# Kernel optimization log

Measured on AMD Instinct MI355X. Metric: run time of the kernel, lower is better.

## Reference

```python
import jax, jax.numpy as jnp
import numpy as np

BATCH, SEQ, H, N = 8, 4096, 512, 64
DT_MIN, DT_MAX = 1e-3, 1e-1


def setup_inputs() -> dict:
    key = jax.random.key(0)
    k1, k2, k3, k4, k5 = jax.random.split(key, 5)
    n = jnp.arange(N, dtype=jnp.float32)
    # HiPPO-LegS diagonal: A[n,n] = -(n+1) -> log|diag(A)| = log(n+1)
    A_log = jnp.broadcast_to(jnp.log(n + 1.0), (H, N))
    Bv = jnp.broadcast_to(jnp.sqrt(2.0 * n + 1.0), (H, N))
    C = jax.random.normal(k1, (H, N), dtype=jnp.float32) * 0.01
    D = jnp.ones((H,), dtype=jnp.float32)
    log_dt = jax.random.uniform(k2, (H,), dtype=jnp.float32) * (
        np.log(DT_MAX) - np.log(DT_MIN)) + np.log(DT_MIN)
    # reverse-direction params (bidirectional)
    A_log_r = A_log
    B_r = Bv
    C_r = jax.random.normal(k3, (H, N), dtype=jnp.float32) * 0.01
    # out_bi Linear: weight [H, 2H], bias [H]
    W_bi = jax.random.normal(k4, (H, 2 * H), dtype=jnp.float32) / np.sqrt(2.0 * H)
    b_bi = jnp.zeros((H,), dtype=jnp.float32)
    u = jax.random.normal(k5, (BATCH, SEQ, H), dtype=jnp.float32)
    return {"u": u, "A_log": A_log, "Bv": Bv, "C": C, "D": D,
            "log_dt": log_dt, "A_log_r": A_log_r, "B_r": B_r, "C_r": C_r,
            "W_bi": W_bi, "b_bi": b_bi}


def _conv(u, A_log, Bp, Cp, D, log_dt):
    """Diagonal SSM as FFT convolution. u: [B, L, H]."""
    L = u.shape[1]
    dt = jnp.exp(log_dt)                      # [H]
    eA = jnp.exp(A_log)                       # [H, N]
    A_bar = jnp.exp(-dt[:, None] * eA)        # [H, N]
    B_bar = (A_bar - 1.0) / (-eA) * Bp        # [H, N]
    # log-space power kernel: A_bar^k = exp(k * log A_bar)
    logA = jnp.log(jnp.clip(A_bar, 1e-30, None))
    ks = jnp.arange(L, dtype=u.dtype)
    pows = jnp.exp(ks[None, None, :] * logA[:, :, None])   # [H, N, L]
    K = jnp.einsum('dn,dnl->dl', Cp * B_bar, pows)          # [H, L]
    n_fft = 2 * L
    u_f = jnp.fft.rfft(u, n=n_fft, axis=1)                  # [B, L+1, H] complex
    K_f = jnp.fft.rfft(K, n=n_fft, axis=-1)                 # [H, L+1]
    y = jnp.fft.irfft(u_f * K_f.T[None], n=n_fft, axis=1)[:, :L, :]
    return y + u * D


def reference(u, A_log, Bv, C, D, log_dt, A_log_r, B_r, C_r, W_bi, b_bi):
    y = _conv(u, A_log, Bv, C, D, log_dt)
    yr = jnp.flip(_conv(jnp.flip(u, 1), A_log_r, B_r, C_r, D, log_dt), 1)
    ycat = jnp.concatenate([y, yr], axis=-1)                # [B, L, 2H]
    return ycat @ W_bi.T + b_bi
```

## Files before the change

### kernel.cpp

```cpp
#include <hip/hip_runtime.h>
#include <hip/hip_bf16.h>
#include <stdint.h>

#define L_SEQ  4096
#define H_DIM  512
#define N_ST   64
#define N_B    8
#define N_CH   16
#define T_CH   256
#define K_GEMM 1024

typedef float  f32x4  __attribute__((ext_vector_type(4)));
typedef __bf16 bf16x8 __attribute__((ext_vector_type(8)));
typedef __bf16 bf16x4 __attribute__((ext_vector_type(4)));
typedef unsigned short u16x8 __attribute__((ext_vector_type(8)));
typedef unsigned long long ull;

#define GLOAD16(g, l) __builtin_amdgcn_global_load_lds( \
    (const __attribute__((address_space(1))) void*)(g), \
    (__attribute__((address_space(3))) void*)(l), 16, 0, 0)

__global__ __launch_bounds__(256) void k_ut(
    const float* __restrict__ u, __bf16* __restrict__ ut,
    const float* __restrict__ W, __bf16* __restrict__ Wbf,
    const float* __restrict__ A_log, const float* __restrict__ Bv,
    const float* __restrict__ C, const float* __restrict__ log_dt,
    const float* __restrict__ A_log_r, const float* __restrict__ B_r,
    const float* __restrict__ C_r,
    float* __restrict__ kk, float* __restrict__ pLG,
    float* __restrict__ pCB, float* __restrict__ pPW)
{
    __shared__ float tl[32][65];
    __shared__ float scb[64], slg[64];
    int blk = blockIdx.x;
    int t = threadIdx.x;

    if (blk >= 8192) {
        int dirh = blk - 8192;
        int dir  = dirh >> 9, h = dirh & 511;
        int d = t;
        if (d < 64) {
            int n = d;
            float dt = expf(log_dt[h]);
            const float* Al = dir ? A_log_r : A_log;
            const float* Bp = dir ? B_r    : Bv;
            const float* Cp = dir ? C_r    : C;
            float eA = expf(Al[h * N_ST + n]);
            float Ab = expf(-dt * eA);
            float Bb = (1.0f - Ab) / eA * Bp[h * N_ST + n];
            float cb = Cp[h * N_ST + n] * Bb;
            float lg = -dt * eA * 1.44269504088896f;
            scb[n] = cb; slg[n] = lg;
            pCB[dirh * 64 + n] = cb;
            pLG[dirh * 64 + n] = lg;
            pPW[dirh * 64 + n] = expf(-dt * eA * (float)T_CH);
        }
        __syncthreads();
        float s = 0.f;
        #pragma unroll
        for (int n = 0; n < 64; ++n) s += scb[n] * exp2f((float)d * slg[n]);
        kk[dirh * 256 + d] = s;
        return;
    }

    int lt = blk & 127, ht = (blk >> 7) & 7, b = blk >> 10;
    int ho = t & 63, li = t >> 6;
    #pragma unroll
    for (int it = 0; it < 8; ++it) {
        int l = it * 4 + li;
        tl[l][ho] = u[(size_t)(b * L_SEQ + lt * 32 + l) * H_DIM + ht * 64 + ho];
    }
    if (blk < 2048) {
        int i = blk * 256 + t;
        Wbf[i] = (__bf16)W[i];
    }
    __syncthreads();
    int hh = t >> 2, lrun = (t & 3) * 8;
    bf16x8 v;
    #pragma unroll
    for (int i = 0; i < 8; ++i) v[i] = (__bf16)tl[lrun + i][hh];
    *(bf16x8*)(ut + (size_t)(ht * 64 + hh) * 32768 + b * 4096 + lt * 32 + lrun) = v;
}

__global__ __launch_bounds__(512, 2) void k_state(
    const __bf16* __restrict__ ut, const float* __restrict__ pLG,
    const float* __restrict__ pPW, __bf16* __restrict__ S2)
{
    __shared__ __bf16 uts[16384];
    int h = blockIdx.x;
    int t = threadIdx.x;
    int lane = t & 63, w = t >> 6;
    int lr = lane & 15, lg = lane >> 4;
    int dir = w >> 2, mtile = w & 3;

    float s = pLG[(size_t)(dir * 512 + h) * 64 + mtile * 16 + lr];
    f32x4 pw4 = *(const f32x4*)(pPW + (size_t)(dir * 512 + h) * 64 + mtile * 16 + lg * 4);

    bf16x8 Mf[8];
    #pragma unroll
    for (int kk = 0; kk < 8; ++kk) {
        #pragma unroll
        for (int jj = 0; jj < 8; ++jj) {
            int j = kk * 32 + lg * 8 + jj;
            float e = dir ? (float)j : (float)(255 - j);
            Mf[kk][jj] = (__bf16)exp2f(e * s);
        }
    }

    for (int hf = 0; hf < 2; ++hf) {
        if (hf) __syncthreads();
        #pragma unroll
        for (int i = 0; i < 4; ++i) {
            int chunk = i * 512 + t;
            int col   = chunk >> 5;
            int l8    = (chunk & 31) << 3;
            int l8s   = l8 ^ ((col & 7) << 3);
            GLOAD16(ut + (size_t)h * 32768 + (hf * 64 + col) * 256 + l8s,
                    (char*)uts + chunk * 16);
        }
        __syncthreads();

        #pragma unroll
        for (int ntile = 0; ntile < 4; ++ntile) {
            f32x4 acc = {};
            #pragma unroll
            for (int kk = 0; kk < 8; ++kk) {
                int col = ntile * 16 + lr;
                bf16x8 bv = *(const bf16x8*)((char*)uts + col * 512
                             + (((kk * 4 + lg) ^ (col & 7)) << 4));
                acc = __builtin_amdgcn_mfma_f32_16x16x32_bf16(Mf[kk], bv, acc, 0, 0, 0);
            }
            f32x4 X;
            if (dir == 0) {
                f32x4 incl = acc;
                float p0 = pw4[0], p1 = pw4[1], p2 = pw4[2], p3 = pw4[3];
                #pragma unroll
                for (int st = 1; st <= 8; st <<= 1) {
                    float u0 = __shfl(incl[0], (lane - st) & 63);
                    float u1 = __shfl(incl[1], (lane - st) & 63);
                    float u2 = __shfl(incl[2], (lane - st) & 63);
                    float u3 = __shfl(incl[3], (lane - st) & 63);
                    if (lr >= st) {
                        incl[0] = fmaf(p0, u0, incl[0]);
                        incl[1] = fmaf(p1, u1, incl[1]);
                        incl[2] = fmaf(p2, u2, incl[2]);
                        incl[3] = fmaf(p3, u3, incl[3]);
                    }
                    p0 *= p0; p1 *= p1; p2 *= p2; p3 *= p3;
                }
                #pragma unroll
                for (int r = 0; r < 4; ++r) {
                    float sh = __shfl(incl[r], (lane - 1) & 63);
                    X[r] = (lr == 0) ? 0.f : sh;
                }
            } else {
                f32x4 incl = acc;
                float p0 = pw4[0], p1 = pw4[1], p2 = pw4[2], p3 = pw4[3];
                #pragma unroll
                for (int st = 1; st <= 8; st <<= 1) {
                    float u0 = __shfl(incl[0], (lane + st) & 63);
                    float u1 = __shfl(incl[1], (lane + st) & 63);
                    float u2 = __shfl(incl[2], (lane + st) & 63);
                    float u3 = __shfl(incl[3], (lane + st) & 63);
                    if (lr <= 15 - st) {
                        incl[0] = fmaf(p0, u0, incl[0]);
                        incl[1] = fmaf(p1, u1, incl[1]);
                        incl[2] = fmaf(p2, u2, incl[2]);
                        incl[3] = fmaf(p3, u3, incl[3]);
                    }
                    p0 *= p0; p1 *= p1; p2 *= p2; p3 *= p3;
                }
                #pragma unroll
                for (int r = 0; r < 4; ++r) {
                    float sh = __shfl(incl[r], (lane + 1) & 63);
                    X[r] = (lr == 15) ? 0.f : sh;
                }
            }
            int colg = hf * 64 + ntile * 16 + lr;
            int nq   = mtile * 4 + lg;
            bf16x4 o;
            #pragma unroll
            for (int r = 0; r < 4; ++r) o[r] = (__bf16)X[r];
            *(bf16x4*)(S2 + ((size_t)((dir * 512 + h) * 16 + nq) * 128 + colg) * 4) = o;
        }
    }
}

template<int DIR>
__device__ __forceinline__ void conv_body(
    int h, int t,
    const float* __restrict__ kk, const float* __restrict__ pLG,
    const float* __restrict__ pCB, const float* __restrict__ Dv,
    const __bf16* __restrict__ ut, const __bf16* __restrict__ S,
    __bf16* __restrict__ ycT,
    __bf16* uts, ull* kkq8, float* slg, float* scb)
{
    int dirh = DIR * 512 + h;
    int lane = t & 63, w = t >> 6;
    int lr = lane & 15, lg = lane >> 4;

    unsigned short* asc = (unsigned short*)uts;
    for (int i = t; i < 548; i += 512) {
        int d = DIR ? (i - 272) : (271 - i);
        float kv = (d >= 0 && d < 256) ? kk[dirh * 256 + d] : 0.f;
        asc[i] = __builtin_bit_cast(unsigned short, (__bf16)kv);
    }
    if (t < 64)       slg[t]      = pLG[dirh * 64 + t];
    else if (t < 128) scb[t - 64] = pCB[dirh * 64 + (t - 64)];
    __syncthreads();
    for (int i = t; i < 544; i += 512)
        kkq8[i] = (ull)asc[i] | ((ull)asc[i+1] << 16) | ((ull)asc[i+2] << 32)
                | ((ull)asc[i+3] << 48);
    __syncthreads();

    bf16x8 gvv[2][2];
    #pragma unroll
    for (int nt = 0; nt < 2; ++nt)
        #pragma unroll
        for (int mf = 0; mf < 2; ++mf) {
            int rt = mf ? (15 - w) : w;
            int l  = rt * 16 + lr;
            float e = DIR ? (float)(256 - l) : (float)(l + 1);
            #pragma unroll
            for (int j = 0; j < 8; ++j) {
                int n = nt * 32 + lg * 8 + j;
                gvv[nt][mf][j] = (__bf16)(scb[n] * exp2f(e * slg[n]));
            }
        }

    float Dh = Dv[h];
    const ull* kq = kkq8;

    #pragma unroll
    for (int hf = 0; hf < 2; ++hf)
        #pragma unroll
        for (int i = 0; i < 4; ++i) {
            int chunk = i * 512 + t;
            int col   = chunk >> 5;
            int l8    = (chunk & 31) << 3;
            int l8s   = l8 ^ ((col & 7) << 3);
            GLOAD16(ut + (size_t)h * 32768 + (hf * 64 + col) * 256 + l8s,
                    (char*)uts + hf * 32768 + chunk * 16);
        }
    asm volatile("s_waitcnt vmcnt(4)" ::: "memory");
    __builtin_amdgcn_sched_barrier(0);
    __builtin_amdgcn_s_barrier();
    __builtin_amdgcn_sched_barrier(0);

    #pragma unroll
    for (int hf = 0; hf < 2; ++hf) {
        if (hf) __syncthreads();
        char* ub = (char*)uts + hf * 32768;

        f32x4 acc[2][4] = {};

        #pragma unroll
        for (int mf = 0; mf < 2; ++mf) {
            int rt  = mf ? (15 - w) : w;
            int jlo = DIR ? (rt >> 1) : 0;
            int jhi = DIR ? 8 : ((rt >> 1) + 1);
            int sb  = (DIR ? 272 : 271) + lg * 8 - rt * 16 - lr;
            for (int jt = jlo; jt < jhi; ++jt) {
                bf16x8 bv[4];
                #pragma unroll
                for (int n = 0; n < 4; ++n) {
                    int col = n * 16 + lr;
                    bv[n] = *(const bf16x8*)(ub + col * 512
                              + (((jt * 4 + lg) ^ (col & 7)) << 4));
                }
                int si = sb + jt * 32;
                ull lo = kq[si], hi = kq[si + 4];
                bf16x8 av;
                ((ull*)&av)[0] = lo; ((ull*)&av)[1] = hi;
                #pragma unroll
                for (int n = 0; n < 4; ++n)
                    acc[mf][n] = __builtin_amdgcn_mfma_f32_16x16x32_bf16(av, bv[n], acc[mf][n], 0, 0, 0);
            }
        }

        #pragma unroll
        for (int nt = 0; nt < 2; ++nt) {
            bf16x8 bs[4];
            #pragma unroll
            for (int n = 0; n < 4; ++n) {
                int colg = (hf * 4 + n) * 16 + lr;
                int nq0  = nt * 8 + lg * 2;
                const __bf16* sp = S + ((size_t)((DIR * 512 + h) * 16 + nq0) * 128 + colg) * 4;
                bf16x4 s0 = *(const bf16x4*)(sp);
                bf16x4 s1 = *(const bf16x4*)(sp + 512);
                #pragma unroll
                for (int j = 0; j < 4; ++j) { bs[n][j] = s0[j]; bs[n][4 + j] = s1[j]; }
            }
            #pragma unroll
            for (int mf = 0; mf < 2; ++mf)
                #pragma unroll
                for (int n = 0; n < 4; ++n)
                    acc[mf][n] = __builtin_amdgcn_mfma_f32_16x16x32_bf16(gvv[nt][mf], bs[n], acc[mf][n], 0, 0, 0);
        }

        #pragma unroll
        for (int mf = 0; mf < 2; ++mf) {
            int rt = mf ? (15 - w) : w;
            int l0 = rt * 16 + lg * 4;
            #pragma unroll
            for (int n = 0; n < 4; ++n) {
                int col = n * 16 + lr;
                bf16x4 uv = *(const bf16x4*)(ub + col * 512
                             + ((((l0 >> 3) ^ (col & 7)) << 4) | ((l0 & 7) * 2)));
                bf16x4 o;
                #pragma unroll
                for (int r = 0; r < 4; ++r)
                    o[r] = (__bf16)(acc[mf][n][r] + Dh * (float)uv[r]);
                *(bf16x4*)(ycT + (size_t)dirh * 32768 + (hf * 64 + col) * 256 + l0) = o;
            }
        }
    }
}

__global__ __launch_bounds__(512, 4) void k_conv(
    const float* __restrict__ kk, const float* __restrict__ pLG,
    const float* __restrict__ pCB, const float* __restrict__ Dv,
    const __bf16* __restrict__ ut, const __bf16* __restrict__ S,
    __bf16* __restrict__ ycT)
{
    __shared__ __bf16 uts[32768];
    __shared__ ull kkq8[544];
    __shared__ float slg[64], scb[64];
    int h = blockIdx.x & 511;
    int t = threadIdx.x;
    if (blockIdx.x >> 9)
        conv_body<1>(h, t, kk, pLG, pCB, Dv, ut, S, ycT, uts, kkq8, slg, scb);
    else
        conv_body<0>(h, t, kk, pLG, pCB, Dv, ut, S, ycT, uts, kkq8, slg, scb);
}

__global__ __launch_bounds__(256, 2) void k_gemm(
    const __bf16* __restrict__ ycT, const __bf16* __restrict__ B,
    const float* __restrict__ bias, float* __restrict__ out)
{
    __shared__ __bf16 As[2][4][128][8];
    __shared__ __bf16 Bs[3][256][32];
    int t  = threadIdx.x;
    int l  = t & 63, w = t >> 6;
    int lr = l & 15, lg = l >> 4;
    int bid   = blockIdx.y * 2 + blockIdx.x;
    int swzid = (bid & 7) * 64 + (bid >> 3);
    int mBase = (swzid >> 1) * 128;
    int nBase = (swzid & 1) * 256;
    int wr = (w >> 1) * 64, wc = (w & 1) * 128;

    int sT  = t & 15;
    int sp  = t >> 4;
    int swz  = (sT & 7) << 4;
    int kgrp = sp >> 2;
    int keb  = (sp & 3) * 4;

    f32x4 acc[4][8] = {};
    const __bf16* aptr = ycT + mBase + sT * 8;

#define STAGE_A(abuf, va0, va1) do { \
    char* AsB_ = (char*)&As[0][0][0][0] + (abuf) * 8192; \
    _Pragma("unroll") \
    for (int i = 0; i < 8; ++i) { \
        unsigned v_ = (unsigned)(unsigned short)(va0)[i] \
                    | ((unsigned)(unsigned short)(va1)[i] << 16); \
        int off_ = ((kgrp * 128 + sT * 8 + i) * 16 + keb) ^ swz; \
        *(unsigned*)(AsB_ + off_) = v_; \
    } } while (0)

#define STAGE_B(bbuf, kt_) do { \
    char* BsB_ = (char*)&Bs[0][0][0] + (bbuf) * 16384; \
    _Pragma("unroll") \
    for (int i = 0; i < 4; ++i) { \
        int chunk_ = i * 256 + t; \
        int row_ = chunk_ >> 2, kq_ = chunk_ & 3; \
        int kqs_ = kq_ ^ ((row_ >> 1) & 3); \
        GLOAD16(B + (size_t)(nBase + row_) * K_GEMM + (kt_) + kqs_ * 8, \
                BsB_ + chunk_ * 16); \
    } } while (0)

#define COMPUTE(abuf, bbuf) do { \
    char* AsB_ = (char*)&As[0][0][0][0] + (abuf) * 8192; \
    char* BsB_ = (char*)&Bs[0][0][0] + (bbuf) * 16384; \
    bf16x8 af_[4], bfv_[8]; \
    _Pragma("unroll") \
    for (int m = 0; m < 4; ++m) { \
        int row_ = wr + m * 16 + lr; \
        int off_ = ((lg * 128 + row_) * 16) ^ (((row_ >> 3) & 7) << 4); \
        af_[m] = *(const bf16x8*)(AsB_ + off_); \
    } \
    _Pragma("unroll") \
    for (int n = 0; n < 8; ++n) { \
        int row_ = wc + n * 16 + lr; \
        bfv_[n] = *(const bf16x8*)(BsB_ + row_ * 64 \
                    + ((lg * 16) ^ (((row_ >> 1) & 3) << 4))); \
    } \
    _Pragma("unroll") \
    for (int m = 0; m < 4; ++m) \
        _Pragma("unroll") \
        for (int n = 0; n < 8; ++n) \
            acc[m][n] = __builtin_amdgcn_mfma_f32_16x16x32_bf16(af_[m], bfv_[n], acc[m][n], 0, 0, 0); \
    } while (0)

    u16x8 a0 = *(const u16x8*)(aptr + (size_t)(2 * sp) * 32768);
    u16x8 a1 = *(const u16x8*)(aptr + (size_t)(2 * sp + 1) * 32768);
    STAGE_B(0, 0);
    STAGE_B(1, 32);

    int ab = 0, cb = 0, sb = 2;
    for (int kt = 0; kt <= 928; kt += 32) {
        STAGE_A(ab, a0, a1);
        a0 = *(const u16x8*)(aptr + (size_t)(kt + 32 + 2 * sp) * 32768);
        a1 = *(const u16x8*)(aptr + (size_t)(kt + 32 + 2 * sp + 1) * 32768);
        STAGE_B(sb, kt + 64);
        asm volatile("s_waitcnt vmcnt(10) lgkmcnt(0)" ::: "memory");
        __builtin_amdgcn_sched_barrier(0);
        __builtin_amdgcn_s_barrier();
        __builtin_amdgcn_sched_barrier(0);
        COMPUTE(ab, cb);
        __builtin_amdgcn_s_barrier();
        ab ^= 1;
        cb = (cb == 2) ? 0 : cb + 1;
        sb = (sb == 2) ? 0 : sb + 1;
    }
    STAGE_A(ab, a0, a1);
    a0 = *(const u16x8*)(aptr + (size_t)(992 + 2 * sp) * 32768);
    a1 = *(const u16x8*)(aptr + (size_t)(992 + 2 * sp + 1) * 32768);
    asm volatile("s_waitcnt vmcnt(6) lgkmcnt(0)" ::: "memory");
    __builtin_amdgcn_sched_barrier(0);
    __builtin_amdgcn_s_barrier();
    __builtin_amdgcn_sched_barrier(0);
    COMPUTE(ab, cb);
    __builtin_amdgcn_s_barrier();
    ab ^= 1;
    cb = (cb == 2) ? 0 : cb + 1;
    STAGE_A(ab, a0, a1);
    asm volatile("s_waitcnt vmcnt(0) lgkmcnt(0)" ::: "memory");
    __builtin_amdgcn_sched_barrier(0);
    __builtin_amdgcn_s_barrier();
    __builtin_amdgcn_sched_barrier(0);
    COMPUTE(ab, cb);

#undef STAGE_A
#undef STAGE_B
#undef COMPUTE

    #pragma unroll
    for (int n = 0; n < 8; ++n) {
        int colg = nBase + wc + n * 16 + lr;
        float bv = bias[colg];
        #pragma unroll
        for (int m = 0; m < 4; ++m) {
            int rowg = mBase + wr + m * 16 + lg * 4;
            #pragma unroll
            for (int r = 0; r < 4; ++r)
                out[(size_t)(rowg + r) * H_DIM + colg] = acc[m][n][r] + bv;
        }
    }
}

extern "C" void kernel_launch(void* const* d_in, const int* in_sizes, int n_in,
                              void* d_out, int out_size, void* d_ws, size_t ws_size,
                              hipStream_t stream)
{
    const float* u       = (const float*)d_in[0];
    const float* A_log   = (const float*)d_in[1];
    const float* Bv      = (const float*)d_in[2];
    const float* C       = (const float*)d_in[3];
    const float* D       = (const float*)d_in[4];
    const float* log_dt  = (const float*)d_in[5];
    const float* A_log_r = (const float*)d_in[6];
    const float* B_r     = (const float*)d_in[7];
    const float* C_r     = (const float*)d_in[8];
    const float* W_bi    = (const float*)d_in[9];
    const float* b_bi    = (const float*)d_in[10];
    float* out = (float*)d_out;

    char* ws = (char*)d_ws;
    float* pCB  = (float*)(ws + 0x040000);
    float* pPW  = (float*)(ws + 0x080000);
    float* pLG  = (float*)(ws + 0x0C0000);
    float* kk   = (float*)(ws + 0x100000);
    __bf16* Wbf = (__bf16*)(ws + 0x200000);
    __bf16* S   = (__bf16*)(ws + 0x300000);
    __bf16* ut  = (__bf16*)(ws + 0x1300000);
    __bf16* ycT = (__bf16*)(ws + 0x3300000);

    k_ut   <<<9216, 256, 0, stream>>>(u, ut, W_bi, Wbf,
                                      A_log, Bv, C, log_dt, A_log_r, B_r, C_r,
                                      kk, pLG, pCB, pPW);
    k_state<<<512,  512, 0, stream>>>(ut, pLG, pPW, S);
    k_conv <<<1024, 512, 0, stream>>>(kk, pLG, pCB, D, ut, S, ycT);
    dim3 g(2, 256);
    k_gemm <<<g,    256, 0, stream>>>(ycT, Wbf, b_bi, out);
}
```

Before: 128.5 us.

## Halve conv LDS staging buffer and load u halves sequentially for higher occupancy

The conv kernel now stages only one 64-column half of the u tile in shared memory (32 KB instead of 64 KB) and reloads the second half after the first half is processed. The kernel-coefficient scratch gets its own small LDS array instead of aliasing the u buffer, so the first u load can be issued at kernel start. Launch bounds rise from 4 to 8 blocks per multiprocessor to use the freed LDS. In exchange, the second half's global load is no longer overlapped with compute within a block and adds extra barriers; latency hiding must come from more resident blocks.

```diff
diff --git a/kernel.cpp b/kernel.cpp
--- a/kernel.cpp
+++ b/kernel.cpp
@@ -193,13 +193,22 @@
     const float* __restrict__ pCB, const float* __restrict__ Dv,
     const __bf16* __restrict__ ut, const __bf16* __restrict__ S,
     __bf16* __restrict__ ycT,
-    __bf16* uts, ull* kkq8, float* slg, float* scb)
+    __bf16* uts, ull* kkq8, unsigned short* asc, float* slg, float* scb)
 {
     int dirh = DIR * 512 + h;
     int lane = t & 63, w = t >> 6;
     int lr = lane & 15, lg = lane >> 4;
 
-    unsigned short* asc = (unsigned short*)uts;
+    #pragma unroll
+    for (int i = 0; i < 4; ++i) {
+        int chunk = i * 512 + t;
+        int col   = chunk >> 5;
+        int l8    = (chunk & 31) << 3;
+        int l8s   = l8 ^ ((col & 7) << 3);
+        GLOAD16(ut + (size_t)h * 32768 + col * 256 + l8s,
+                (char*)uts + chunk * 16);
+    }
+
     for (int i = t; i < 548; i += 512) {
         int d = DIR ? (i - 272) : (271 - i);
         float kv = (d >= 0 && d < 256) ? kk[dirh * 256 + d] : 0.f;
@@ -207,11 +216,13 @@
     }
     if (t < 64)       slg[t]      = pLG[dirh * 64 + t];
     else if (t < 128) scb[t - 64] = pCB[dirh * 64 + (t - 64)];
-    __syncthreads();
+    asm volatile("s_waitcnt lgkmcnt(0)" ::: "memory");
+    __builtin_amdgcn_sched_barrier(0);
+    __builtin_amdgcn_s_barrier();
+    __builtin_amdgcn_sched_barrier(0);
     for (int i = t; i < 544; i += 512)
         kkq8[i] = (ull)asc[i] | ((ull)asc[i+1] << 16) | ((ull)asc[i+2] << 32)
                 | ((ull)asc[i+3] << 48);
-    __syncthreads();
 
     bf16x8 gvv[2][2];
     #pragma unroll
@@ -231,26 +242,14 @@
     float Dh = Dv[h];
     const ull* kq = kkq8;
 
-    #pragma unroll
-    for (int hf = 0; hf < 2; ++hf)
-        #pragma unroll
-        for (int i = 0; i < 4; ++i) {
-            int chunk = i * 512 + t;
-            int col   = chunk >> 5;
-            int l8    = (chunk & 31) << 3;
-            int l8s   = l8 ^ ((col & 7) << 3);
-            GLOAD16(ut + (size_t)h * 32768 + (hf * 64 + col) * 256 + l8s,
-                    (char*)uts + hf * 32768 + chunk * 16);
-        }
-    asm volatile("s_waitcnt vmcnt(4)" ::: "memory");
+    asm volatile("s_waitcnt vmcnt(0) lgkmcnt(0)" ::: "memory");
     __builtin_amdgcn_sched_barrier(0);
     __builtin_amdgcn_s_barrier();
     __builtin_amdgcn_sched_barrier(0);
 
     #pragma unroll
     for (int hf = 0; hf < 2; ++hf) {
-        if (hf) __syncthreads();
-        char* ub = (char*)uts + hf * 32768;
+        char* ub = (char*)uts;
 
         f32x4 acc[2][4] = {};
 
@@ -314,24 +313,45 @@
                 *(bf16x4*)(ycT + (size_t)dirh * 32768 + (hf * 64 + col) * 256 + l0) = o;
             }
         }
+
+        if (hf == 0) {
+            asm volatile("s_waitcnt lgkmcnt(0)" ::: "memory");
+            __builtin_amdgcn_sched_barrier(0);
+            __builtin_amdgcn_s_barrier();
+            __builtin_amdgcn_sched_barrier(0);
+            #pragma unroll
+            for (int i = 0; i < 4; ++i) {
+                int chunk = i * 512 + t;
+                int col   = chunk >> 5;
+                int l8    = (chunk & 31) << 3;
+                int l8s   = l8 ^ ((col & 7) << 3);
+                GLOAD16(ut + (size_t)h * 32768 + (64 + col) * 256 + l8s,
+                        (char*)uts + chunk * 16);
+            }
+            asm volatile("s_waitcnt vmcnt(0)" ::: "memory");
+            __builtin_amdgcn_sched_barrier(0);
+            __builtin_amdgcn_s_barrier();
+            __builtin_amdgcn_sched_barrier(0);
+        }
     }
 }
 
-__global__ __launch_bounds__(512, 4) void k_conv(
+__global__ __launch_bounds__(512, 8) void k_conv(
     const float* __restrict__ kk, const float* __restrict__ pLG,
     const float* __restrict__ pCB, const float* __restrict__ Dv,
     const __bf16* __restrict__ ut, const __bf16* __restrict__ S,
     __bf16* __restrict__ ycT)
 {
-    __shared__ __bf16 uts[32768];
+    __shared__ __bf16 uts[16384];
     __shared__ ull kkq8[544];
+    __shared__ unsigned short asc[548];
     __shared__ float slg[64], scb[64];
     int h = blockIdx.x & 511;
     int t = threadIdx.x;
     if (blockIdx.x >> 9)
-        conv_body<1>(h, t, kk, pLG, pCB, Dv, ut, S, ycT, uts, kkq8, slg, scb);
+        conv_body<1>(h, t, kk, pLG, pCB, Dv, ut, S, ycT, uts, kkq8, asc, slg, scb);
     else
-        conv_body<0>(h, t, kk, pLG, pCB, Dv, ut, S, ycT, uts, kkq8, slg, scb);
+        conv_body<0>(h, t, kk, pLG, pCB, Dv, ut, S, ycT, uts, kkq8, asc, slg, scb);
 }
 
 __global__ __launch_bounds__(256, 2) void k_gemm(
```

After: 227.7 us. +77.1%, slower.
